# Optimization experiments

Measured on AMD Instinct MI355X. Metric: run time of the kernel, lower is better.

Reference implementation:

```python
import jax, jax.numpy as jnp
import numpy as np

SCALE = 128.0          # GriddingDistance scale
GRID_MIN = -64.0       # floor(min coord) for points in (-64, 64)
R = 128                # voxels per axis = ceil(max) - floor(min)
G = R * R * R          # flattened grid size per sample

# 8 trilinear corner offsets (8, 3)
_CORNERS = jnp.array([[i, j, k] for i in (0, 1) for j in (0, 1) for k in (0, 1)], dtype=jnp.int32)


def _gridding(cloud):
    """Trilinear scatter of (b, n, 3) scaled points into (b, G) voxel grid.

    Mirrors gridding.forward: per point, weight each of the 8 surrounding
    voxel corners by prod(1 - |p - corner|) and scatter-add into the grid.
    """
    b, n, _ = cloud.shape
    p = cloud - GRID_MIN                     # shift to [0, R)
    x0f = jnp.floor(p)
    d = p - x0f                              # (b, n, 3) fractional offsets
    x0 = x0f.astype(jnp.int32)
    idx = jnp.clip(x0[:, :, None, :] + _CORNERS, 0, R - 1)      # (b, n, 8, 3)
    # corner weight: d for the +1 corner, (1 - d) for the base corner
    w = jnp.where(_CORNERS[None, None] == 1, d[:, :, None, :], 1.0 - d[:, :, None, :])
    w = w.prod(axis=-1)                      # (b, n, 8)
    flat = (idx[..., 0] * R + idx[..., 1]) * R + idx[..., 2]    # (b, n, 8)
    flat = flat + jnp.arange(b, dtype=jnp.int32)[:, None, None] * G
    grid = jnp.zeros(b * G, dtype=cloud.dtype).at[flat.reshape(-1)].add(w.reshape(-1))
    return grid.reshape(b, G)


def setup_inputs() -> dict:
    key = jax.random.key(0)
    k1, k2 = jax.random.split(key)
    # normalized clouds in (-0.49, 0.49) so scaled points stay inside the grid
    pred = (jax.random.uniform(k1, (8, 65536, 3), dtype=jnp.float32) - 0.5) * 0.98
    gt = (jax.random.uniform(k2, (8, 65536, 3), dtype=jnp.float32) - 0.5) * 0.98
    return {"pred_cloud": pred, "gt_cloud": gt}


def reference(pred_cloud, gt_cloud):
    pred_grid = _gridding(pred_cloud * SCALE)
    gt_grid = _gridding(gt_cloud * SCALE)
    return pred_grid, gt_grid
```

## Files before the change

kernel.cpp:

```cpp
#include <hip/hip_runtime.h>


#define RES   128
#define GRIDG (RES * RES * RES)
#define NSLAB 16
#define NRX   16
#define NREG  256
#define NBIN  (NSLAB * NREG)
#define CAPB  640
#define PTS_PER_BLOCK 1024

__device__ __forceinline__ int clampi(int v) {
    return v < 0 ? 0 : (v > RES - 1 ? RES - 1 : v);
}


__global__ __launch_bounds__(256) void place_kernel(
    const float* __restrict__ pred, const float* __restrict__ gt,
    unsigned* __restrict__ cursor,
    float4* __restrict__ bins,
    int npts, int nblkPerSlab)
{
    __shared__ unsigned cnt[NREG];
    __shared__ unsigned curs[NREG];

    const int gblk = blockIdx.x;
    const int slab = gblk / nblkPerSlab;
    const int blk  = gblk - slab * nblkPerSlab;
    const float* cloud = (slab < 8) ? pred : gt;
    const float* cbase = cloud + (size_t)(slab & 7) * npts * 3
                               + (size_t)blk * PTS_PER_BLOCK * 3;

    const int t = threadIdx.x;
    cnt[t] = 0;
    __syncthreads();

    float px[4], py[4], pz[4];
    bool valid[4];
    const bool fullBlock = ((blk + 1) * PTS_PER_BLOCK) <= npts;

    if (fullBlock) {
        const float4* b4 = (const float4*)cbase;
        const float4 f0 = b4[3 * t + 0];
        const float4 f1 = b4[3 * t + 1];
        const float4 f2 = b4[3 * t + 2];
        px[0] = f0.x; py[0] = f0.y; pz[0] = f0.z;
        px[1] = f0.w; py[1] = f1.x; pz[1] = f1.y;
        px[2] = f1.z; py[2] = f1.w; pz[2] = f2.x;
        px[3] = f2.y; py[3] = f2.z; pz[3] = f2.w;
#pragma unroll
        for (int k = 0; k < 4; ++k) {
            valid[k] = true;
            px[k] = fmaf(px[k], 128.0f, 64.0f);
            py[k] = fmaf(py[k], 128.0f, 64.0f);
            pz[k] = fmaf(pz[k], 128.0f, 64.0f);
        }
    } else {
#pragma unroll
        for (int k = 0; k < 4; ++k) {
            const int jj = 4 * t + k;
            valid[k] = (blk * PTS_PER_BLOCK + jj < npts);
            if (valid[k]) {
                px[k] = fmaf(cbase[(size_t)jj * 3 + 0], 128.0f, 64.0f);
                py[k] = fmaf(cbase[(size_t)jj * 3 + 1], 128.0f, 64.0f);
                pz[k] = fmaf(cbase[(size_t)jj * 3 + 2], 128.0f, 64.0f);
            }
        }
    }

#pragma unroll
    for (int k = 0; k < 4; ++k) {
        if (!valid[k]) continue;
        const int ix = (int)floorf(px[k]), iy = (int)floorf(py[k]);
        const int rx0 = clampi(ix) >> 3, rx1 = clampi(ix + 1) >> 3;
        const int ry0 = clampi(iy) >> 3, ry1 = clampi(iy + 1) >> 3;
        for (int a = rx0; a <= rx1; ++a)
            for (int b = ry0; b <= ry1; ++b)
                atomicAdd(&cnt[(a << 4) | b], 1u);
    }
    __syncthreads();

    {
        const unsigned c = cnt[t];
        unsigned base = 0;
        if (c) base = atomicAdd(&cursor[slab * NREG + t], c);
        curs[t] = base;
    }
    __syncthreads();

#pragma unroll
    for (int k = 0; k < 4; ++k) {
        if (!valid[k]) continue;
        const float x = px[k], y = py[k], z = pz[k];
        const int ix = (int)floorf(x), iy = (int)floorf(y);
        const int rx0 = clampi(ix) >> 3, rx1 = clampi(ix + 1) >> 3;
        const int ry0 = clampi(iy) >> 3, ry1 = clampi(iy + 1) >> 3;
        for (int a = rx0; a <= rx1; ++a)
            for (int b = ry0; b <= ry1; ++b) {
                const int r = (a << 4) | b;
                const unsigned slot = atomicAdd(&curs[r], 1u);
                if (slot < CAPB)
                    bins[(size_t)(slab * NREG + r) * CAPB + slot] =
                        make_float4(x, y, z, 0.0f);
            }
    }
}


__global__ __launch_bounds__(256) void accum_kernel(
    const float4* __restrict__ bins, const unsigned* __restrict__ cursor,
    float* __restrict__ out)
{
    __shared__ __align__(16) float vox[8 * 8 * 128];

    const int bin  = blockIdx.x;
    const int slab = bin >> 8;
    const int reg  = bin & 255;
    const int rx = reg >> 4, ry = reg & 15;

    unsigned n = cursor[bin];
    if (n > CAPB) n = CAPB;

    float4* v4 = (float4*)vox;
    for (int i = threadIdx.x; i < 2048; i += 256) v4[i] = make_float4(0, 0, 0, 0);
    __syncthreads();

    const float4* seg = bins + (size_t)bin * CAPB;
    for (unsigned i = threadIdx.x; i < n; i += 256) {
        const float4 e = seg[i];
        const float x = e.x, y = e.y, z = e.z;
        const float xf = floorf(x), yf = floorf(y), zf = floorf(z);
        const float dx = x - xf, dy = y - yf, dz = z - zf;
        const int ix = (int)xf, iy = (int)yf, iz = (int)zf;
        const int x0 = clampi(ix), x1 = clampi(ix + 1);
        const int y0 = clampi(iy), y1 = clampi(iy + 1);
        const int z0 = clampi(iz), z1 = clampi(iz + 1);
        const float wx0 = 1.0f - dx, wy0 = 1.0f - dy, wz0 = 1.0f - dz;

#pragma unroll
        for (int sx = 0; sx < 2; ++sx) {
            const int cx = sx ? x1 : x0;
            if ((cx >> 3) != rx) continue;
            const float wx = sx ? dx : wx0;
#pragma unroll
            for (int sy = 0; sy < 2; ++sy) {
                const int cy = sy ? y1 : y0;
                if ((cy >> 3) != ry) continue;
                const float wxy = wx * (sy ? dy : wy0);
                const int base = ((cx & 7) << 10) | ((cy & 7) << 7);
                atomicAdd(&vox[base + z0], wxy * wz0);
                atomicAdd(&vox[base + z1], wxy * dz);
            }
        }
    }
    __syncthreads();

    float* gp = out + (size_t)slab * GRIDG
              + ((size_t)rx << 17) + ((size_t)ry << 10);
    for (int v = threadIdx.x; v < 2048; v += 256) {
        const int l   = v << 2;
        const int lx  = l >> 10;
        const int rem = l & 1023;
        *(float4*)(gp + ((size_t)lx << 14) + rem) = v4[v];
    }
}


__global__ __launch_bounds__(256) void gridding_scatter_kernel(
    const float* __restrict__ cloud, float* __restrict__ grid, int n)
{
    const int j = blockIdx.x * blockDim.x + threadIdx.x;
    if (j >= n) return;
    const int b = blockIdx.y;
    const size_t pt = (size_t)b * n + j;

    const float x = fmaf(cloud[pt * 3 + 0], 128.0f, 64.0f);
    const float y = fmaf(cloud[pt * 3 + 1], 128.0f, 64.0f);
    const float z = fmaf(cloud[pt * 3 + 2], 128.0f, 64.0f);
    const float xf = floorf(x), yf = floorf(y), zf = floorf(z);
    const float dx = x - xf, dy = y - yf, dz = z - zf;
    const int ix = (int)xf, iy = (int)yf, iz = (int)zf;
    const int x0 = clampi(ix), x1 = clampi(ix + 1);
    const int y0 = clampi(iy), y1 = clampi(iy + 1);
    const int z0 = clampi(iz), z1 = clampi(iz + 1);
    const float wx0 = 1.0f - dx, wy0 = 1.0f - dy, wz0 = 1.0f - dz;

    float* gp = grid + (size_t)b * GRIDG;
    const int bx0 = x0 << 14, bx1 = x1 << 14;
    const int by0 = y0 << 7,  by1 = y1 << 7;
    atomicAdd(gp + (bx0 + by0 + z0), wx0 * wy0 * wz0);
    atomicAdd(gp + (bx0 + by0 + z1), wx0 * wy0 * dz);
    atomicAdd(gp + (bx0 + by1 + z0), wx0 * dy * wz0);
    atomicAdd(gp + (bx0 + by1 + z1), wx0 * dy * dz);
    atomicAdd(gp + (bx1 + by0 + z0), dx * wy0 * wz0);
    atomicAdd(gp + (bx1 + by0 + z1), dx * wy0 * dz);
    atomicAdd(gp + (bx1 + by1 + z0), dx * dy * wz0);
    atomicAdd(gp + (bx1 + by1 + z1), dx * dy * dz);
}


extern "C" void kernel_launch(void* const* d_in, const int* in_sizes, int n_in,
                              void* d_out, int out_size, void* d_ws, size_t ws_size,
                              hipStream_t stream) {
    const float* pred = (const float*)d_in[0];
    const float* gt   = (const float*)d_in[1];
    float* out = (float*)d_out;

    const int bsz  = 8;
    const int npts = in_sizes[0] / (bsz * 3);

    const size_t cursorBytes = (size_t)NBIN * sizeof(unsigned);
    const size_t binsBytes   = (size_t)NBIN * CAPB * sizeof(float4);
    const size_t needWs      = cursorBytes + binsBytes;

    if (ws_size >= needWs) {
        unsigned* cursor = (unsigned*)d_ws;
        float4* bins = (float4*)((char*)d_ws + cursorBytes);

        hipMemsetAsync(cursor, 0, cursorBytes, stream);

        const int nblkPerSlab = (npts + PTS_PER_BLOCK - 1) / PTS_PER_BLOCK;
        place_kernel<<<dim3(NSLAB * nblkPerSlab), dim3(256), 0, stream>>>(
            pred, gt, cursor, bins, npts, nblkPerSlab);
        accum_kernel<<<dim3(NBIN), dim3(256), 0, stream>>>(bins, cursor, out);
    } else {
        hipMemsetAsync(d_out, 0, (size_t)out_size * sizeof(float), stream);
        dim3 block(256);
        dim3 grid((npts + 255) / 256, bsz);
        float* pred_grid = out;
        float* gt_grid   = out + (size_t)bsz * GRIDG;
        gridding_scatter_kernel<<<grid, block, 0, stream>>>(pred, pred_grid, npts);
        gridding_scatter_kernel<<<grid, block, 0, stream>>>(gt,   gt_grid,   npts);
    }
}
```

Before: 188.5 us.

## Replace global bin cursors with fixed per-block sub-bins and nontemporal grid stores

The place kernel no longer counts points then reserves space through global atomics. Each block writes its points into its own fixed-capacity sub-bin (32 slots per region per block) and records a per-block count. This removes the global atomic phase, one barrier and the memset. The accumulate kernel walks a 64x32 slot grid and skips empty slots, and the output grid is written with nontemporal stores. The cost is a fixed per-block capacity that can drop points if a region overflows, and the fast path now requires exactly 64 blocks per slab.

```diff
diff --git a/kernel.cpp b/kernel.cpp
--- a/kernel.cpp
+++ b/kernel.cpp
@@ -4,11 +4,13 @@
 #define RES   128
 #define GRIDG (RES * RES * RES)
 #define NSLAB 16
-#define NRX   16
 #define NREG  256
 #define NBIN  (NSLAB * NREG)
-#define CAPB  640
+#define BPS   64
+#define CAP2  32
 #define PTS_PER_BLOCK 1024
+
+typedef float floatx4 __attribute__((ext_vector_type(4)));
 
 __device__ __forceinline__ int clampi(int v) {
     return v < 0 ? 0 : (v > RES - 1 ? RES - 1 : v);
@@ -17,12 +19,11 @@
 
 __global__ __launch_bounds__(256) void place_kernel(
     const float* __restrict__ pred, const float* __restrict__ gt,
-    unsigned* __restrict__ cursor,
+    unsigned* __restrict__ cnt,
     float4* __restrict__ bins,
     int npts, int nblkPerSlab)
 {
-    __shared__ unsigned cnt[NREG];
-    __shared__ unsigned curs[NREG];
+    __shared__ unsigned lcnt[NREG];
 
     const int gblk = blockIdx.x;
     const int slab = gblk / nblkPerSlab;
@@ -32,7 +33,7 @@
                                + (size_t)blk * PTS_PER_BLOCK * 3;
 
     const int t = threadIdx.x;
-    cnt[t] = 0;
+    lcnt[t] = 0;
     __syncthreads();
 
     float px[4], py[4], pz[4];
@@ -64,30 +65,13 @@
                 px[k] = fmaf(cbase[(size_t)jj * 3 + 0], 128.0f, 64.0f);
                 py[k] = fmaf(cbase[(size_t)jj * 3 + 1], 128.0f, 64.0f);
                 pz[k] = fmaf(cbase[(size_t)jj * 3 + 2], 128.0f, 64.0f);
+            } else {
+                px[k] = py[k] = pz[k] = 0.0f;
             }
         }
     }
 
-#pragma unroll
-    for (int k = 0; k < 4; ++k) {
-        if (!valid[k]) continue;
-        const int ix = (int)floorf(px[k]), iy = (int)floorf(py[k]);
-        const int rx0 = clampi(ix) >> 3, rx1 = clampi(ix + 1) >> 3;
-        const int ry0 = clampi(iy) >> 3, ry1 = clampi(iy + 1) >> 3;
-        for (int a = rx0; a <= rx1; ++a)
-            for (int b = ry0; b <= ry1; ++b)
-                atomicAdd(&cnt[(a << 4) | b], 1u);
-    }
-    __syncthreads();
-
-    {
-        const unsigned c = cnt[t];
-        unsigned base = 0;
-        if (c) base = atomicAdd(&cursor[slab * NREG + t], c);
-        curs[t] = base;
-    }
-    __syncthreads();
-
+    const size_t slabBase = (size_t)slab * NREG * BPS * CAP2;
 #pragma unroll
     for (int k = 0; k < 4; ++k) {
         if (!valid[k]) continue;
@@ -98,36 +82,47 @@
         for (int a = rx0; a <= rx1; ++a)
             for (int b = ry0; b <= ry1; ++b) {
                 const int r = (a << 4) | b;
-                const unsigned slot = atomicAdd(&curs[r], 1u);
-                if (slot < CAPB)
-                    bins[(size_t)(slab * NREG + r) * CAPB + slot] =
+                const unsigned slot = atomicAdd(&lcnt[r], 1u);
+                if (slot < CAP2)
+                    bins[slabBase + ((size_t)r * BPS + blk) * CAP2 + slot] =
                         make_float4(x, y, z, 0.0f);
             }
     }
+    __syncthreads();
+
+    unsigned c = lcnt[t];
+    if (c > CAP2) c = CAP2;
+    cnt[((size_t)slab * NREG + t) * BPS + blk] = c;
 }
 
 
 __global__ __launch_bounds__(256) void accum_kernel(
-    const float4* __restrict__ bins, const unsigned* __restrict__ cursor,
+    const float4* __restrict__ bins, const unsigned* __restrict__ cnt,
     float* __restrict__ out)
 {
     __shared__ __align__(16) float vox[8 * 8 * 128];
+    __shared__ unsigned c[BPS];
 
     const int bin  = blockIdx.x;
     const int slab = bin >> 8;
     const int reg  = bin & 255;
     const int rx = reg >> 4, ry = reg & 15;
-
-    unsigned n = cursor[bin];
-    if (n > CAPB) n = CAPB;
+    const int t = threadIdx.x;
 
     float4* v4 = (float4*)vox;
-    for (int i = threadIdx.x; i < 2048; i += 256) v4[i] = make_float4(0, 0, 0, 0);
-    __syncthreads();
-
-    const float4* seg = bins + (size_t)bin * CAPB;
-    for (unsigned i = threadIdx.x; i < n; i += 256) {
-        const float4 e = seg[i];
+    for (int i = t; i < 2048; i += 256) v4[i] = make_float4(0, 0, 0, 0);
+    if (t < BPS) {
+        unsigned cc = cnt[(size_t)bin * BPS + t];
+        c[t] = cc > CAP2 ? CAP2 : cc;
+    }
+    __syncthreads();
+
+    const float4* seg = bins + (size_t)bin * BPS * CAP2;
+    for (int s = t; s < BPS * CAP2; s += 256) {
+        const int b = s >> 5;
+        const int i = s & 31;
+        if (i >= (int)c[b]) continue;
+        const float4 e = seg[s];
         const float x = e.x, y = e.y, z = e.z;
         const float xf = floorf(x), yf = floorf(y), zf = floorf(z);
         const float dx = x - xf, dy = y - yf, dz = z - zf;
@@ -157,11 +152,13 @@
 
     float* gp = out + (size_t)slab * GRIDG
               + ((size_t)rx << 17) + ((size_t)ry << 10);
-    for (int v = threadIdx.x; v < 2048; v += 256) {
+    const floatx4* lv = (const floatx4*)vox;
+    for (int v = t; v < 2048; v += 256) {
         const int l   = v << 2;
         const int lx  = l >> 10;
         const int rem = l & 1023;
-        *(float4*)(gp + ((size_t)lx << 14) + rem) = v4[v];
+        __builtin_nontemporal_store(lv[v],
+            (floatx4*)(gp + ((size_t)lx << 14) + rem));
     }
 }
 
@@ -209,22 +206,21 @@
     const int bsz  = 8;
     const int npts = in_sizes[0] / (bsz * 3);
 
-    const size_t cursorBytes = (size_t)NBIN * sizeof(unsigned);
-    const size_t binsBytes   = (size_t)NBIN * CAPB * sizeof(float4);
-    const size_t needWs      = cursorBytes + binsBytes;
-
-    if (ws_size >= needWs) {
-        unsigned* cursor = (unsigned*)d_ws;
-        float4* bins = (float4*)((char*)d_ws + cursorBytes);
-
-        hipMemsetAsync(cursor, 0, cursorBytes, stream);
-
-        const int nblkPerSlab = (npts + PTS_PER_BLOCK - 1) / PTS_PER_BLOCK;
+    const int nblkPerSlab = (npts + PTS_PER_BLOCK - 1) / PTS_PER_BLOCK;
+
+    const size_t cntBytes  = (size_t)NBIN * BPS * sizeof(unsigned);
+    const size_t binsBytes = (size_t)NBIN * BPS * CAP2 * sizeof(float4);
+    const size_t needWs    = cntBytes + binsBytes;
+
+    if (ws_size >= needWs && nblkPerSlab == BPS) {
+        unsigned* cnt = (unsigned*)d_ws;
+        float4* bins = (float4*)((char*)d_ws + cntBytes);
+
         place_kernel<<<dim3(NSLAB * nblkPerSlab), dim3(256), 0, stream>>>(
-            pred, gt, cursor, bins, npts, nblkPerSlab);
-        accum_kernel<<<dim3(NBIN), dim3(256), 0, stream>>>(bins, cursor, out);
+            pred, gt, cnt, bins, npts, nblkPerSlab);
+        accum_kernel<<<dim3(NBIN), dim3(256), 0, stream>>>(bins, cnt, out);
     } else {
-        hipMemsetAsync(d_out, 0, (size_t)out_size * sizeof(float), stream);
+        (void)hipMemsetAsync(d_out, 0, (size_t)out_size * sizeof(float), stream);
         dim3 block(256);
         dim3 grid((npts + 255) / 256, bsz);
         float* pred_grid = out;
```

Result: slower. 216.6 us (+14.9%).

## Stage binned points in LDS sorted by region and use nontemporal grid stores

Applied to the files above, without the earlier changes.

The place kernel now runs a block-wide prefix scan over the per-region counts and writes each point copy into a shared-memory staging buffer ordered by region. It then flushes that buffer to the global bins, so each region's entries go out as a contiguous run instead of as scattered float4 writes. The accumulation kernel writes its output tiles with nontemporal stores so the large grid write-back does not pollute the cache. In exchange, the place kernel gains extra barriers for the scan and a 32 KB shared buffer that may cut occupancy. Entries beyond the staging capacity would be silently dropped.

```diff
diff --git a/kernel.cpp b/kernel.cpp
--- a/kernel.cpp
+++ b/kernel.cpp
@@ -4,11 +4,13 @@
 #define RES   128
 #define GRIDG (RES * RES * RES)
 #define NSLAB 16
-#define NRX   16
 #define NREG  256
 #define NBIN  (NSLAB * NREG)
 #define CAPB  640
+#define STAGE_CAP 2048
 #define PTS_PER_BLOCK 1024
+
+typedef float floatx4 __attribute__((ext_vector_type(4)));
 
 __device__ __forceinline__ int clampi(int v) {
     return v < 0 ? 0 : (v > RES - 1 ? RES - 1 : v);
@@ -22,7 +24,10 @@
     int npts, int nblkPerSlab)
 {
     __shared__ unsigned cnt[NREG];
+    __shared__ unsigned scan[NREG];
     __shared__ unsigned curs[NREG];
+    __shared__ unsigned gbase[NREG];
+    __shared__ __align__(16) float4 stage[STAGE_CAP];
 
     const int gblk = blockIdx.x;
     const int slab = gblk / nblkPerSlab;
@@ -64,6 +69,8 @@
                 px[k] = fmaf(cbase[(size_t)jj * 3 + 0], 128.0f, 64.0f);
                 py[k] = fmaf(cbase[(size_t)jj * 3 + 1], 128.0f, 64.0f);
                 pz[k] = fmaf(cbase[(size_t)jj * 3 + 2], 128.0f, 64.0f);
+            } else {
+                px[k] = py[k] = pz[k] = 0.0f;
             }
         }
     }
@@ -80,11 +87,22 @@
     }
     __syncthreads();
 
+    unsigned v = cnt[t];
+    scan[t] = v;
+    __syncthreads();
+    for (int d = 1; d < NREG; d <<= 1) {
+        unsigned add = (t >= d) ? scan[t - d] : 0u;
+        __syncthreads();
+        scan[t] += add;
+        __syncthreads();
+    }
+
     {
         const unsigned c = cnt[t];
         unsigned base = 0;
         if (c) base = atomicAdd(&cursor[slab * NREG + t], c);
-        curs[t] = base;
+        gbase[t] = base;
+        curs[t] = scan[t] - c;
     }
     __syncthreads();
 
@@ -98,11 +116,28 @@
         for (int a = rx0; a <= rx1; ++a)
             for (int b = ry0; b <= ry1; ++b) {
                 const int r = (a << 4) | b;
-                const unsigned slot = atomicAdd(&curs[r], 1u);
-                if (slot < CAPB)
-                    bins[(size_t)(slab * NREG + r) * CAPB + slot] =
-                        make_float4(x, y, z, 0.0f);
+                const unsigned idx = atomicAdd(&curs[r], 1u);
+                if (idx < STAGE_CAP) {
+                    float4 e; e.x = x; e.y = y; e.z = z;
+                    e.w = __int_as_float(r);
+                    stage[idx] = e;
+                }
             }
+    }
+    __syncthreads();
+
+    unsigned total = scan[NREG - 1];
+    if (total > STAGE_CAP) total = STAGE_CAP;
+    const size_t slabBase = (size_t)slab * NREG * CAPB;
+    for (unsigned e = t; e < total; e += 256) {
+        float4 f = stage[e];
+        const int r = __float_as_int(f.w);
+        const unsigned local = e - (scan[r] - cnt[r]);
+        const unsigned gslot = gbase[r] + local;
+        if (gslot < CAPB) {
+            f.w = 0.0f;
+            bins[slabBase + (size_t)r * CAPB + gslot] = f;
+        }
     }
 }
 
@@ -117,16 +152,17 @@
     const int slab = bin >> 8;
     const int reg  = bin & 255;
     const int rx = reg >> 4, ry = reg & 15;
+    const int t = threadIdx.x;
 
     unsigned n = cursor[bin];
     if (n > CAPB) n = CAPB;
 
     float4* v4 = (float4*)vox;
-    for (int i = threadIdx.x; i < 2048; i += 256) v4[i] = make_float4(0, 0, 0, 0);
+    for (int i = t; i < 2048; i += 256) v4[i] = make_float4(0, 0, 0, 0);
     __syncthreads();
 
     const float4* seg = bins + (size_t)bin * CAPB;
-    for (unsigned i = threadIdx.x; i < n; i += 256) {
+    for (unsigned i = t; i < n; i += 256) {
         const float4 e = seg[i];
         const float x = e.x, y = e.y, z = e.z;
         const float xf = floorf(x), yf = floorf(y), zf = floorf(z);
@@ -157,11 +193,13 @@
 
     float* gp = out + (size_t)slab * GRIDG
               + ((size_t)rx << 17) + ((size_t)ry << 10);
-    for (int v = threadIdx.x; v < 2048; v += 256) {
-        const int l   = v << 2;
+    const floatx4* lv = (const floatx4*)vox;
+    for (int i = t; i < 2048; i += 256) {
+        const int l   = i << 2;
         const int lx  = l >> 10;
         const int rem = l & 1023;
-        *(float4*)(gp + ((size_t)lx << 14) + rem) = v4[v];
+        __builtin_nontemporal_store(lv[i],
+            (floatx4*)(gp + ((size_t)lx << 14) + rem));
     }
 }
 
@@ -217,14 +255,14 @@
         unsigned* cursor = (unsigned*)d_ws;
         float4* bins = (float4*)((char*)d_ws + cursorBytes);
 
-        hipMemsetAsync(cursor, 0, cursorBytes, stream);
+        (void)hipMemsetAsync(cursor, 0, cursorBytes, stream);
 
         const int nblkPerSlab = (npts + PTS_PER_BLOCK - 1) / PTS_PER_BLOCK;
         place_kernel<<<dim3(NSLAB * nblkPerSlab), dim3(256), 0, stream>>>(
             pred, gt, cursor, bins, npts, nblkPerSlab);
         accum_kernel<<<dim3(NBIN), dim3(256), 0, stream>>>(bins, cursor, out);
     } else {
-        hipMemsetAsync(d_out, 0, (size_t)out_size * sizeof(float), stream);
+        (void)hipMemsetAsync(d_out, 0, (size_t)out_size * sizeof(float), stream);
         dim3 block(256);
         dim3 grid((npts + 255) / 256, bsz);
         float* pred_grid = out;
```

Measured after the change: 196.1 us. 1.04x slower.
